# Kernel tuning notes

Hardware: AMD Instinct MI355X
Metric: run time of the kernel (lower is better)

## Reference

```python
import jax, jax.numpy as jnp
import numpy as np

WIN = 2
PC = 48
IMG = 128
D = PC * WIN * WIN      # token dim == state dim N == 192
NS = IMG // WIN          # 64
L = NS * NS              # 4096 tokens
BATCH = 2


def setup_inputs() -> dict:
    key = jax.random.key(0)
    ks = jax.random.split(key, 8)
    s = 1.0 / np.sqrt(D)  # nn.Linear default init scale
    x = jax.random.normal(ks[0], (BATCH, PC, IMG, IMG), jnp.float32)
    A_log = jnp.log(jax.random.uniform(ks[1], (D, D), jnp.float32, 1.0, 16.0))
    D_param = jnp.ones((D,), jnp.float32)
    W_B = jax.random.uniform(ks[2], (D, D), jnp.float32, -s, s)
    b_B = jax.random.uniform(ks[3], (D,), jnp.float32, -s, s)
    W_C = jax.random.uniform(ks[4], (D, D), jnp.float32, -s, s)
    b_C = jax.random.uniform(ks[5], (D,), jnp.float32, -s, s)
    W_dt = jax.random.uniform(ks[6], (D, D), jnp.float32, -s, s)
    b_dt = jax.random.uniform(ks[7], (D,), jnp.float32, -s, s)
    return {"x": x, "A_log": A_log, "D_param": D_param, "W_B": W_B, "b_B": b_B,
            "W_C": W_C, "b_C": b_C, "W_dt": W_dt, "b_dt": b_dt}


def _forward(x, A_log, D_param, W_B, b_B, W_C, b_C, W_dt, b_dt):
    Bb, C, H, W = x.shape
    w = WIN
    # unfold into non-overlapping windows -> tokens (B, L, D) with D = C*w*w (channel-major)
    t = x.reshape(Bb, C, H // w, w, W // w, w).transpose(0, 1, 2, 4, 3, 5)
    tokens = t.reshape(Bb, C, -1, w * w).transpose(0, 2, 1, 3).reshape(Bb, -1, D)
    Bm = tokens @ W_B.T + b_B                      # (B, L, D) -> state input proj
    Cm = tokens @ W_C.T + b_C                      # (B, L, D) -> state output proj
    dt = jax.nn.softplus(tokens @ W_dt.T + b_dt)   # module applies softplus once
    # selective_scan_fn applies delta = softplus(delta + delta_bias) again (delta_softplus=True)
    delta = jax.nn.softplus(dt + b_dt)             # (B, L, D)
    A = -jnp.exp(A_log)                            # (D, N) with N == D
    u = tokens                                     # (B, L, D)

    def step(h, inp):
        d_l, u_l, B_l, C_l = inp                   # (B,D) (B,D) (B,N) (B,N)
        dA = jnp.exp(d_l[:, :, None] * A[None])    # (B, D, N)
        h = dA * h + (d_l * u_l)[:, :, None] * B_l[:, None, :]
        y = jnp.einsum('bdn,bn->bd', h, C_l)
        return h, y

    h0 = jnp.zeros((Bb, D, D), x.dtype)
    xs = (delta.transpose(1, 0, 2), u.transpose(1, 0, 2),
          Bm.transpose(1, 0, 2), Cm.transpose(1, 0, 2))
    _, ys = jax.lax.scan(step, h0, xs)             # (L, B, D)
    y = ys.transpose(1, 2, 0)                      # (B, D, L)
    y = y + D_param[None, :, None] * u.transpose(0, 2, 1)
    z = jnp.ones_like(y)                           # z = ones in the module
    y = y * (z * jax.nn.sigmoid(z))                # silu(z) gating
    out = y.reshape(Bb, NS, NS, PC, w, w).transpose(0, 3, 1, 4, 2, 5)
    return out.reshape(Bb, PC, NS * w, NS * w)


def reference(x, A_log, D_param, W_B, b_B, W_C, b_C, W_dt, b_dt):
    return _forward(x, A_log, D_param, W_B, b_B, W_C, b_C, W_dt, b_dt)
```

## Files before the change

kernel.cpp:

```cpp
#include <hip/hip_runtime.h>
#include <hip/hip_bf16.h>
#include <math.h>

#define BB   2
#define PCH  48
#define DD   192
#define NSB  64
#define LL   4096
#define NCH  128
#define LCH  32
#define WUP  12
#define NG   8
#define NCK  24
#define SILU1 0.7310585786300049f

typedef float v2f __attribute__((ext_vector_type(2)));
typedef float v4f __attribute__((ext_vector_type(4)));
typedef __bf16 bf16x8 __attribute__((ext_vector_type(8)));
typedef float f32x4 __attribute__((ext_vector_type(4)));

#if __has_builtin(__builtin_amdgcn_exp2f)
#define EXP2(x) __builtin_amdgcn_exp2f(x)
#else
#define EXP2(x) exp2f(x)
#endif

#if __has_builtin(__builtin_elementwise_fma)
static __device__ __forceinline__ v2f fma2(v2f a, v2f b, v2f c) {
    return __builtin_elementwise_fma(a, b, c);
}
#else
static __device__ __forceinline__ v2f fma2(v2f a, v2f b, v2f c) {
    v2f r; r.x = __builtin_fmaf(a.x, b.x, c.x); r.y = __builtin_fmaf(a.y, b.y, c.y);
    return r;
}
#endif

static __device__ __forceinline__ float softplus_(float x) {
    return fmaxf(x, 0.0f) + log1pf(__expf(-fabsf(x)));
}

static __device__ __forceinline__ unsigned short f2bf(float f) {
    unsigned int u = __builtin_bit_cast(unsigned int, f);
    u += 0x7fffu + ((u >> 16) & 1u);
    return (unsigned short)(u >> 16);
}

__global__ void k_tok(const float* __restrict__ x, float* __restrict__ tokens,
                      const float* __restrict__ A_log, float* __restrict__ A2t,
                      const float* __restrict__ W_B, const float* __restrict__ W_C,
                      const float* __restrict__ W_dt,
                      unsigned short* __restrict__ tok_bf,
                      unsigned short* __restrict__ W_bf) {
    __shared__ float lds[64 * 196];
    int b  = blockIdx.x >> 6;
    int hb = blockIdx.x & 63;
    int tid = threadIdx.x;
    for (int t = blockIdx.x * 256 + tid; t < DD * DD; t += 128 * 256) {
        int n = t / DD, d = t - n * DD;
        A2t[t] = -__expf(A_log[d * DD + n]) * 1.4426950408889634f;
    }
    for (int t = blockIdx.x * 256 + tid; t < 3 * DD * DD; t += 128 * 256) {
        int mat = t / (DD * DD), r = t - mat * DD * DD;
        const float* W = (mat == 0) ? W_B : (mat == 1 ? W_C : W_dt);
        W_bf[t] = f2bf(W[r]);
    }
    for (int idx = tid; idx < 48 * 2 * 128; idx += 256) {
        int c = idx >> 8; int r = idx & 255; int i = r >> 7; int w = r & 127;
        float v = x[((b * 48 + c) * 128 + (hb * 2 + i)) * 128 + w];
        int wb = w >> 1, j = w & 1;
        lds[wb * 196 + c * 4 + i * 2 + j] = v;
    }
    __syncthreads();
    for (int idx = tid; idx < 64 * 192; idx += 256) {
        int wb = idx / 192, d = idx - wb * 192;
        float v = lds[wb * 196 + d];
        size_t o = (size_t)(b * 4096 + hb * 64 + wb) * 192 + d;
        tokens[o] = v;
        tok_bf[o] = f2bf(v);
    }
}

__global__ __launch_bounds__(256) void k_proj(
        const unsigned short* __restrict__ tok_bf,
        const unsigned short* __restrict__ W_bf,
        const float* __restrict__ b_B, const float* __restrict__ b_C,
        const float* __restrict__ b_dt,
        float* __restrict__ Bm, float* __restrict__ Cm,
        float* __restrict__ delta) {
    int tid  = threadIdx.x;
    int lane = tid & 63;
    int wv   = tid >> 6;
    int m0   = blockIdx.x * 16;
    int mat  = blockIdx.y;
    int lrow = lane & 15;
    int koff = (lane >> 4) * 8;

    const unsigned short* ap = tok_bf + (size_t)(m0 + lrow) * 192 + koff;
    bf16x8 a[6];
    #pragma unroll
    for (int k0 = 0; k0 < 6; ++k0)
        a[k0] = *reinterpret_cast<const bf16x8*>(ap + k0 * 32);

    f32x4 acc[3];
    #pragma unroll
    for (int jt = 0; jt < 3; ++jt) {
        #pragma unroll
        for (int r = 0; r < 4; ++r) acc[jt][r] = 0.f;
    }
    #pragma unroll
    for (int jt = 0; jt < 3; ++jt) {
        int j = wv * 48 + jt * 16 + lrow;
        const unsigned short* bp = W_bf + (size_t)(mat * 192 + j) * 192 + koff;
        #pragma unroll
        for (int k0 = 0; k0 < 6; ++k0) {
            bf16x8 bv = *reinterpret_cast<const bf16x8*>(bp + k0 * 32);
            acc[jt] = __builtin_amdgcn_mfma_f32_16x16x32_bf16(a[k0], bv, acc[jt],
                                                              0, 0, 0);
        }
    }

    int col = lane & 15;
    int rb  = (lane >> 4) * 4;
    #pragma unroll
    for (int jt = 0; jt < 3; ++jt) {
        int j = wv * 48 + jt * 16 + col;
        #pragma unroll
        for (int r = 0; r < 4; ++r) {
            int m = m0 + rb + r;
            float z = acc[jt][r];
            size_t o = (size_t)m * 192 + j;
            if (mat == 0)       Bm[o] = z + b_B[j];
            else if (mat == 1)  Cm[o] = z + b_C[j];
            else {
                float bd = b_dt[j];
                delta[o] = softplus_(softplus_(z + bd) + bd);
            }
        }
    }
}

__global__ __launch_bounds__(512, 6) void k_scan(
        const float* __restrict__ delta, const float* __restrict__ tokens,
        const float* __restrict__ Bm, const float* __restrict__ Cm,
        const float* __restrict__ A2t, const float* __restrict__ Dp,
        float* __restrict__ out) {
    __shared__ float ytile[LCH * 65];
    __shared__ float utile[LCH * 65];
    int tid = threadIdx.x;
    for (int i = tid; i < LCH * 65; i += 512) ytile[i] = 0.0f;
    __syncthreads();

    int lane = tid & 63;
    int ng   = tid >> 6;
    int blk  = blockIdx.x;
    int c    = blk & (NCH - 1);
    int rest = blk >> 7;
    int dg   = rest % 3, b = rest / 3;
    int d    = dg * 64 + lane;
    int n0   = ng * NCK;

    v2f A2[NCK / 2], h[NCK / 2];
    #pragma unroll
    for (int p = 0; p < NCK / 2; ++p) {
        A2[p].x = A2t[(n0 + 2 * p) * 192 + d];
        A2[p].y = A2t[(n0 + 2 * p + 1) * 192 + d];
        h[p].x = 0.f; h[p].y = 0.f;
    }

    int l0     = c * LCH;
    int nwarm  = (c == 0) ? 0 : WUP;
    int base   = (b * 4096 + l0 - nwarm) * 192;
    int ubase  = __builtin_amdgcn_readfirstlane(base + n0);
    const float* bp = Bm + ubase;
    const float* cp = Cm + ubase;
    const float* dp = delta + base + d;
    const float* up = tokens + base + d;

    float dlt = dp[0], uv = up[0];
    int s = 0;
    #pragma unroll 4
    for (int t = 0; t < nwarm; ++t, ++s) {
        float dn = dp[(s + 1) * 192], un = up[(s + 1) * 192];
        const v4f* B4 = (const v4f*)(bp + s * 192);
        v4f bq[NCK / 4];
        #pragma unroll
        for (int q = 0; q < NCK / 4; ++q) bq[q] = B4[q];
        float du = dlt * uv;
        v2f dlt2; dlt2.x = dlt; dlt2.y = dlt;
        v2f du2;  du2.x = du;   du2.y = du;
        #pragma unroll
        for (int q = 0; q < NCK / 4; ++q) {
            v2f blo = __builtin_shufflevector(bq[q], bq[q], 0, 1);
            v2f bhi = __builtin_shufflevector(bq[q], bq[q], 2, 3);
            v2f e0 = dlt2 * A2[2 * q];
            v2f e1 = dlt2 * A2[2 * q + 1];
            v2f dA0; dA0.x = EXP2(e0.x); dA0.y = EXP2(e0.y);
            v2f dA1; dA1.x = EXP2(e1.x); dA1.y = EXP2(e1.y);
            h[2 * q]     = fma2(dA0, h[2 * q],     du2 * blo);
            h[2 * q + 1] = fma2(dA1, h[2 * q + 1], du2 * bhi);
        }
        dlt = dn; uv = un;
    }
    #pragma unroll 4
    for (int t = 0; t < LCH; ++t, ++s) {
        float dn = dp[(s + 1) * 192], un = up[(s + 1) * 192];
        if (ng == 0) utile[t * 65 + lane] = uv;
        const v4f* B4 = (const v4f*)(bp + s * 192);
        const v4f* C4 = (const v4f*)(cp + s * 192);
        v4f bq[NCK / 4], cq[NCK / 4];
        #pragma unroll
        for (int q = 0; q < NCK / 4; ++q) { bq[q] = B4[q]; cq[q] = C4[q]; }
        float du = dlt * uv;
        v2f dlt2; dlt2.x = dlt; dlt2.y = dlt;
        v2f du2;  du2.x = du;   du2.y = du;
        v2f acc2; acc2.x = 0.f; acc2.y = 0.f;
        #pragma unroll
        for (int q = 0; q < NCK / 4; ++q) {
            v2f blo = __builtin_shufflevector(bq[q], bq[q], 0, 1);
            v2f bhi = __builtin_shufflevector(bq[q], bq[q], 2, 3);
            v2f clo = __builtin_shufflevector(cq[q], cq[q], 0, 1);
            v2f chi = __builtin_shufflevector(cq[q], cq[q], 2, 3);
            v2f e0 = dlt2 * A2[2 * q];
            v2f e1 = dlt2 * A2[2 * q + 1];
            v2f dA0; dA0.x = EXP2(e0.x); dA0.y = EXP2(e0.y);
            v2f dA1; dA1.x = EXP2(e1.x); dA1.y = EXP2(e1.y);
            h[2 * q]     = fma2(dA0, h[2 * q],     du2 * blo);
            h[2 * q + 1] = fma2(dA1, h[2 * q + 1], du2 * bhi);
            acc2 = fma2(h[2 * q],     clo, acc2);
            acc2 = fma2(h[2 * q + 1], chi, acc2);
        }
        atomicAdd(&ytile[t * 65 + lane], acc2.x + acc2.y);
        dlt = dn; uv = un;
    }
    __syncthreads();

    #pragma unroll 1
    for (int idx = tid; idx < LCH * 64; idx += 512) {
        int dd = idx >> 5, t = idx & (LCH - 1);
        int de = dg * 64 + dd;
        int q  = de / 3, rem = de - 3 * q;
        int l  = l0 + t;
        int inner = rem * 4096 + l;
        int a2 = inner / 192;
        int m  = inner - 192 * a2;
        int pc = m >> 2, oi = (m >> 1) & 1, oj = m & 1;
        float val = (ytile[t * 65 + dd] + Dp[de] * utile[t * 65 + dd]) * SILU1;
        out[((size_t)((b * 48 + pc) * 128 + 2 * q + oi)) * 128 + 2 * a2 + oj] =
            val;
    }
}

extern "C" void kernel_launch(void* const* d_in, const int* in_sizes, int n_in,
                              void* d_out, int out_size, void* d_ws, size_t ws_size,
                              hipStream_t stream) {
    const float* x     = (const float*)d_in[0];
    const float* A_log = (const float*)d_in[1];
    const float* Dp    = (const float*)d_in[2];
    const float* W_B   = (const float*)d_in[3];
    const float* b_B   = (const float*)d_in[4];
    const float* W_C   = (const float*)d_in[5];
    const float* b_C   = (const float*)d_in[6];
    const float* W_dt  = (const float*)d_in[7];
    const float* b_dt  = (const float*)d_in[8];
    float* out = (float*)d_out;

    const size_t TOK = (size_t)BB * LL * DD;
    float* ws = (float*)d_ws;
    float* tokens = ws;
    float* Bm     = tokens + TOK;
    float* Cm     = Bm + TOK;
    float* delta  = Cm + TOK;
    float* A2t    = delta + TOK;
    unsigned short* tok_bf = (unsigned short*)(A2t + (size_t)DD * DD);
    unsigned short* W_bf   = tok_bf + TOK;

    k_tok<<<dim3(BB * NSB), dim3(256), 0, stream>>>(x, tokens, A_log, A2t,
                                                    W_B, W_C, W_dt, tok_bf, W_bf);
    k_proj<<<dim3(512, 3), dim3(256), 0, stream>>>(tok_bf, W_bf, b_B, b_C, b_dt,
                                                   Bm, Cm, delta);
    k_scan<<<dim3(BB * 3 * NCH), dim3(512), 0, stream>>>(delta, tokens, Bm, Cm,
                                                         A2t, Dp, out);
}
```

Baseline: 121.9 us.

## Fuse token unfolding into projection GEMM and split weight prep kernel

Token unfolding from the image now happens inside the projection kernel through LDS, and bf16 conversion is done in registers. This removes the separate bf16 token buffer and its global round trip. Each block now computes all three projections (B, C, dt) for its 16 rows, so the x gather is done once per row tile instead of three times. Weight conversion and A precompute move to a small prep kernel. The trade-off is fewer projection blocks (512 instead of 1536) with more serial MFMA work per wave.

```diff
diff --git a/kernel.cpp b/kernel.cpp
--- a/kernel.cpp
+++ b/kernel.cpp
@@ -46,94 +46,92 @@
     return (unsigned short)(u >> 16);
 }
 
-__global__ void k_tok(const float* __restrict__ x, float* __restrict__ tokens,
-                      const float* __restrict__ A_log, float* __restrict__ A2t,
-                      const float* __restrict__ W_B, const float* __restrict__ W_C,
-                      const float* __restrict__ W_dt,
-                      unsigned short* __restrict__ tok_bf,
-                      unsigned short* __restrict__ W_bf) {
-    __shared__ float lds[64 * 196];
-    int b  = blockIdx.x >> 6;
-    int hb = blockIdx.x & 63;
-    int tid = threadIdx.x;
-    for (int t = blockIdx.x * 256 + tid; t < DD * DD; t += 128 * 256) {
+__global__ void k_prep(const float* __restrict__ A_log, float* __restrict__ A2t,
+                       const float* __restrict__ W_B, const float* __restrict__ W_C,
+                       const float* __restrict__ W_dt,
+                       unsigned short* __restrict__ W_bf) {
+    int t = blockIdx.x * 256 + threadIdx.x;
+    if (t < DD * DD) {
         int n = t / DD, d = t - n * DD;
         A2t[t] = -__expf(A_log[d * DD + n]) * 1.4426950408889634f;
     }
-    for (int t = blockIdx.x * 256 + tid; t < 3 * DD * DD; t += 128 * 256) {
+    if (t < 3 * DD * DD) {
         int mat = t / (DD * DD), r = t - mat * DD * DD;
         const float* W = (mat == 0) ? W_B : (mat == 1 ? W_C : W_dt);
         W_bf[t] = f2bf(W[r]);
     }
-    for (int idx = tid; idx < 48 * 2 * 128; idx += 256) {
-        int c = idx >> 8; int r = idx & 255; int i = r >> 7; int w = r & 127;
-        float v = x[((b * 48 + c) * 128 + (hb * 2 + i)) * 128 + w];
-        int wb = w >> 1, j = w & 1;
-        lds[wb * 196 + c * 4 + i * 2 + j] = v;
-    }
-    __syncthreads();
-    for (int idx = tid; idx < 64 * 192; idx += 256) {
-        int wb = idx / 192, d = idx - wb * 192;
-        float v = lds[wb * 196 + d];
-        size_t o = (size_t)(b * 4096 + hb * 64 + wb) * 192 + d;
-        tokens[o] = v;
-        tok_bf[o] = f2bf(v);
-    }
-}
-
-__global__ __launch_bounds__(256) void k_proj(
-        const unsigned short* __restrict__ tok_bf,
+}
+
+__global__ __launch_bounds__(256) void k_tokproj(
+        const float* __restrict__ x,
         const unsigned short* __restrict__ W_bf,
         const float* __restrict__ b_B, const float* __restrict__ b_C,
         const float* __restrict__ b_dt,
+        float* __restrict__ tokens,
         float* __restrict__ Bm, float* __restrict__ Cm,
         float* __restrict__ delta) {
+    __shared__ float tokL[16 * 200];
     int tid  = threadIdx.x;
     int lane = tid & 63;
     int wv   = tid >> 6;
-    int m0   = blockIdx.x * 16;
-    int mat  = blockIdx.y;
+    int m0 = blockIdx.x * 16;
+    int b  = m0 >> 12;
+    int l0 = m0 & 4095;
+    int hb  = l0 >> 6;
+    int wb0 = l0 & 63;
+
+    for (int idx = tid; idx < 3072; idx += 256) {
+        int r  = idx >> 5;
+        int c  = r >> 1, i = r & 1;
+        int wq = idx & 31;
+        int wbp = wq >> 1, j = wq & 1;
+        float v = x[((size_t)(b * 48 + c) * 128 + 2 * hb + i) * 128
+                    + 2 * wb0 + wq];
+        tokL[wbp * 200 + c * 4 + i * 2 + j] = v;
+    }
+    __syncthreads();
+
+    for (int idx = tid; idx < 16 * 192; idx += 256) {
+        int wbp = idx / 192, d = idx - wbp * 192;
+        tokens[(size_t)(m0 + wbp) * 192 + d] = tokL[wbp * 200 + d];
+    }
+
     int lrow = lane & 15;
     int koff = (lane >> 4) * 8;
-
-    const unsigned short* ap = tok_bf + (size_t)(m0 + lrow) * 192 + koff;
     bf16x8 a[6];
     #pragma unroll
-    for (int k0 = 0; k0 < 6; ++k0)
-        a[k0] = *reinterpret_cast<const bf16x8*>(ap + k0 * 32);
-
-    f32x4 acc[3];
-    #pragma unroll
-    for (int jt = 0; jt < 3; ++jt) {
-        #pragma unroll
-        for (int r = 0; r < 4; ++r) acc[jt][r] = 0.f;
-    }
-    #pragma unroll
-    for (int jt = 0; jt < 3; ++jt) {
-        int j = wv * 48 + jt * 16 + lrow;
-        const unsigned short* bp = W_bf + (size_t)(mat * 192 + j) * 192 + koff;
-        #pragma unroll
-        for (int k0 = 0; k0 < 6; ++k0) {
-            bf16x8 bv = *reinterpret_cast<const bf16x8*>(bp + k0 * 32);
-            acc[jt] = __builtin_amdgcn_mfma_f32_16x16x32_bf16(a[k0], bv, acc[jt],
-                                                              0, 0, 0);
-        }
+    for (int k0 = 0; k0 < 6; ++k0) {
+        const float* src = &tokL[lrow * 200 + koff + k0 * 32];
+        #pragma unroll
+        for (int e = 0; e < 8; ++e)
+            a[k0][e] = (__bf16)src[e];
     }
 
     int col = lane & 15;
     int rb  = (lane >> 4) * 4;
     #pragma unroll
-    for (int jt = 0; jt < 3; ++jt) {
-        int j = wv * 48 + jt * 16 + col;
+    for (int jt = 0; jt < 9; ++jt) {
+        int jj = wv * 144 + jt * 16;
+        const unsigned short* bp = W_bf + (size_t)(jj + lrow) * 192 + koff;
+        f32x4 acc;
+        #pragma unroll
+        for (int r = 0; r < 4; ++r) acc[r] = 0.f;
+        #pragma unroll
+        for (int k0 = 0; k0 < 6; ++k0) {
+            bf16x8 bv = *reinterpret_cast<const bf16x8*>(bp + k0 * 32);
+            acc = __builtin_amdgcn_mfma_f32_16x16x32_bf16(a[k0], bv, acc, 0, 0, 0);
+        }
+        int mat = jj / 192;
+        int jl  = jj - mat * 192 + col;
         #pragma unroll
         for (int r = 0; r < 4; ++r) {
             int m = m0 + rb + r;
-            float z = acc[jt][r];
-            size_t o = (size_t)m * 192 + j;
-            if (mat == 0)       Bm[o] = z + b_B[j];
-            else if (mat == 1)  Cm[o] = z + b_C[j];
+            float z = acc[r];
+            size_t o = (size_t)m * 192 + jl;
+            if (mat == 0)       Bm[o] = z + b_B[jl];
+            else if (mat == 1)  Cm[o] = z + b_C[jl];
             else {
-                float bd = b_dt[j];
+                float bd = b_dt[jl];
                 delta[o] = softplus_(softplus_(z + bd) + bd);
             }
         }
@@ -272,13 +270,12 @@
     float* Cm     = Bm + TOK;
     float* delta  = Cm + TOK;
     float* A2t    = delta + TOK;
-    unsigned short* tok_bf = (unsigned short*)(A2t + (size_t)DD * DD);
-    unsigned short* W_bf   = tok_bf + TOK;
-
-    k_tok<<<dim3(BB * NSB), dim3(256), 0, stream>>>(x, tokens, A_log, A2t,
-                                                    W_B, W_C, W_dt, tok_bf, W_bf);
-    k_proj<<<dim3(512, 3), dim3(256), 0, stream>>>(tok_bf, W_bf, b_B, b_C, b_dt,
-                                                   Bm, Cm, delta);
+    unsigned short* W_bf = (unsigned short*)(A2t + (size_t)DD * DD);
+
+    k_prep<<<dim3((3 * DD * DD + 255) / 256), dim3(256), 0, stream>>>(
+        A_log, A2t, W_B, W_C, W_dt, W_bf);
+    k_tokproj<<<dim3(512), dim3(256), 0, stream>>>(x, W_bf, b_B, b_C, b_dt,
+                                                   tokens, Bm, Cm, delta);
     k_scan<<<dim3(BB * 3 * NCH), dim3(512), 0, stream>>>(delta, tokens, Bm, Cm,
                                                          A2t, Dp, out);
 }
```

Measured after the change: 123.2 us. Within noise of the previous version (+1.0%).
